# Kernel tuning notes

Measured on AMD Instinct MI355X. Metric: run time of the kernel, lower is better.

Reference implementation:

```python
import jax, jax.numpy as jnp
import numpy as np

E = 256  # embed_dim (hardcoded in source module)
H = 4    # n_head
D = E // H
SEQ = 32768


def setup_inputs() -> dict:
    key = jax.random.key(0)
    ks = jax.random.split(key, 5)
    x = jax.random.normal(ks[0], (SEQ, E), dtype=jnp.float32)
    in_proj_weight = jax.random.normal(ks[1], (3 * E, E), dtype=jnp.float32) * (1.0 / np.sqrt(E))
    in_proj_bias = jax.random.normal(ks[2], (3 * E,), dtype=jnp.float32) * 0.02
    out_proj_weight = jax.random.normal(ks[3], (E, E), dtype=jnp.float32) * (1.0 / np.sqrt(E))
    out_proj_bias = jax.random.normal(ks[4], (E,), dtype=jnp.float32) * 0.02
    return {
        "x": x,
        "in_proj_weight": in_proj_weight,
        "in_proj_bias": in_proj_bias,
        "out_proj_weight": out_proj_weight,
        "out_proj_bias": out_proj_bias,
    }


def reference(x, in_proj_weight, in_proj_bias, out_proj_weight, out_proj_bias):
    # QKV projections (q uses only the first token of x: single-query decode attention)
    Wq, Wk, Wv = in_proj_weight[:E], in_proj_weight[E:2 * E], in_proj_weight[2 * E:]
    bq, bk, bv = in_proj_bias[:E], in_proj_bias[E:2 * E], in_proj_bias[2 * E:]
    q = x[:1] @ Wq.T + bq            # [1, E]
    k = x @ Wk.T + bk                # [S, E]
    v = x @ Wv.T + bv                # [S, E]

    qh = q.reshape(H, D)             # [H, D] (single query)
    kh = k.reshape(-1, H, D)         # [S, H, D]
    vh = v.reshape(-1, H, D)         # [S, H, D]

    scale = 1.0 / np.sqrt(D).astype(np.float32)
    scores = jnp.einsum("hd,shd->hs", qh, kh) * scale   # [H, S]
    attn = jax.nn.softmax(scores, axis=-1)                # [H, S]
    ctx = jnp.einsum("hs,shd->hd", attn, vh)             # [H, D]

    out = ctx.reshape(1, E) @ out_proj_weight.T + out_proj_bias  # [1, E]
    return out
```

## Files before the change

### kernel.cpp

```cpp
#include <hip/hip_runtime.h>
#include <hip/hip_cooperative_groups.h>
namespace cg = cooperative_groups;

#define S 32768
#define NBLK 256


__device__ __forceinline__ float dot4(float4 a, float4 b) {
  return a.x * b.x + a.y * b.y + a.z * b.z + a.w * b.w;
}

__device__ __forceinline__ void phaseA(const float* __restrict__ x, const float* __restrict__ W,
                                       const float* __restrict__ inb, const float* __restrict__ Wout,
                                       float* __restrict__ kq, float* __restrict__ c4,
                                       float* __restrict__ M2, float* sh, int bid, int t) {
  const int lane = t & 63, w = t >> 6;
  if (bid < 16) {
    float* xs = sh;
    float* qls = sh + 256;
    float* red = sh + 320;
    const int h = bid >> 2, qt = bid & 3;
    if (t < 256) xs[t] = x[t];
    __syncthreads();
    const float4 xv = *(const float4*)&xs[lane * 4];
#pragma unroll
    for (int k = 0; k < 8; ++k) {
      const int eloc = w * 8 + k;
      const int row = h * 64 + eloc;
      float4 wv = *(const float4*)&W[(size_t)row * 256 + lane * 4];
      float p = dot4(wv, xv);
#pragma unroll
      for (int m = 1; m < 64; m <<= 1) p += __shfl_xor(p, m);
      if (lane == 0) qls[eloc] = p + inb[row];
    }
    __syncthreads();
    const int cl = t & 63, ds = t >> 6;
    float acc = 0.f;
#pragma unroll
    for (int d2 = 0; d2 < 8; ++d2) {
      const int d = ds * 8 + d2;
      acc += W[(size_t)(256 + h * 64 + d) * 256 + qt * 64 + cl] * qls[d];
    }
    red[ds * 64 + cl] = acc;
    __syncthreads();
    if (ds == 0) {
      float s = 0.f;
#pragma unroll
      for (int i = 0; i < 8; ++i) s += red[i * 64 + cl];
      kq[h * 256 + qt * 64 + cl] = s;
    }
    if (qt == 0 && t < 64) {
      float v = qls[t] * inb[256 + h * 64 + t];
#pragma unroll
      for (int m = 1; m < 64; m <<= 1) v += __shfl_xor(v, m);
      if (t == 0) c4[h] = v;
    }
  } else if (bid < 144) {
    float* wout_t = sh;
    const int b2 = bid - 16;
    const int tile = b2 >> 1, sub = b2 & 1;
    const int h = tile >> 4, e0 = (tile & 15) * 16 + sub * 8;
    {
      const int e = t >> 6, d = t & 63;
      wout_t[e * 64 + d] = Wout[(size_t)(e0 + e) * 256 + h * 64 + d];
    }
    __syncthreads();
    const int c = t & 255, eh = t >> 8;
    float acc[4] = {0.f, 0.f, 0.f, 0.f};
#pragma unroll 8
    for (int d = 0; d < 64; ++d) {
      const float wv = W[(size_t)(512 + h * 64 + d) * 256 + c];
#pragma unroll
      for (int e = 0; e < 4; ++e) acc[e] += wv * wout_t[(eh * 4 + e) * 64 + d];
    }
#pragma unroll
    for (int e = 0; e < 4; ++e)
      M2[(size_t)(e0 + eh * 4 + e) * 1024 + h * 256 + c] = acc[e];
  }
}

__device__ __forceinline__ float bscore(float4 xv, float4 kq0, float4 kq1, float4 kq2,
                                        float4 kq3, float c4v, int lane) {
  float p0 = dot4(xv, kq0), p1 = dot4(xv, kq1), p2 = dot4(xv, kq2), p3 = dot4(xv, kq3);
  const bool b1 = (lane & 2) != 0;
  float keep0 = b1 ? p2 : p0, send0 = b1 ? p0 : p2;
  keep0 += __shfl_xor(send0, 2);
  float keep1 = b1 ? p3 : p1, send1 = b1 ? p1 : p3;
  keep1 += __shfl_xor(send1, 2);
  const bool b0 = (lane & 1) != 0;
  float vv = b0 ? keep1 : keep0, sv = b0 ? keep0 : keep1;
  vv += __shfl_xor(sv, 1);
  vv += __shfl_xor(vv, 4);
  vv += __shfl_xor(vv, 8);
  vv += __shfl_xor(vv, 16);
  vv += __shfl_xor(vv, 32);
  return (vv + c4v) * 0.125f;
}

__device__ __forceinline__ void phaseB(const float* __restrict__ x, const float* __restrict__ kq,
                                       const float* __restrict__ c4, float* __restrict__ ypart,
                                       float* __restrict__ mpart, float* __restrict__ lpart,
                                       float* sh, int bid, int t) {
  float* yls = sh;
  float* sml = sh + 8192;
  float* sll = sh + 8224;
  const int lane = t & 63, w = t >> 6;
  const int hme = lane & 3;
  const float4 kq0 = *(const float4*)&kq[0 * 256 + lane * 4];
  const float4 kq1 = *(const float4*)&kq[1 * 256 + lane * 4];
  const float4 kq2 = *(const float4*)&kq[2 * 256 + lane * 4];
  const float4 kq3 = *(const float4*)&kq[3 * 256 + lane * 4];
  const float c4v = c4[hme];

  const int r0 = bid * 128 + w * 16;
  float4 xvA[8], xvB[8];
#pragma unroll
  for (int r = 0; r < 8; ++r)
    xvA[r] = *(const float4*)&x[(size_t)(r0 + r) * 256 + lane * 4];
#pragma unroll
  for (int r = 0; r < 8; ++r)
    xvB[r] = *(const float4*)&x[(size_t)(r0 + 8 + r) * 256 + lane * 4];

  float vA[8];
#pragma unroll
  for (int r = 0; r < 8; ++r) vA[r] = bscore(xvA[r], kq0, kq1, kq2, kq3, c4v, lane);
  float m = vA[0];
#pragma unroll
  for (int r = 1; r < 8; ++r) m = fmaxf(m, vA[r]);

  float l = 0.f;
  float4 a[4];
#pragma unroll
  for (int k = 0; k < 4; ++k) a[k] = (float4){0.f, 0.f, 0.f, 0.f};
#pragma unroll
  for (int r = 0; r < 8; ++r) {
    const float e0 = __expf(vA[r] - m);
    l += e0;
    const float e1 = __shfl_xor(e0, 1);
    const float e2 = __shfl_xor(e0, 2);
    const float e3 = __shfl_xor(e0, 3);
    a[0].x += e0 * xvA[r].x; a[0].y += e0 * xvA[r].y; a[0].z += e0 * xvA[r].z; a[0].w += e0 * xvA[r].w;
    a[1].x += e1 * xvA[r].x; a[1].y += e1 * xvA[r].y; a[1].z += e1 * xvA[r].z; a[1].w += e1 * xvA[r].w;
    a[2].x += e2 * xvA[r].x; a[2].y += e2 * xvA[r].y; a[2].z += e2 * xvA[r].z; a[2].w += e2 * xvA[r].w;
    a[3].x += e3 * xvA[r].x; a[3].y += e3 * xvA[r].y; a[3].z += e3 * xvA[r].z; a[3].w += e3 * xvA[r].w;
  }

  float vB[8];
#pragma unroll
  for (int r = 0; r < 8; ++r) vB[r] = bscore(xvB[r], kq0, kq1, kq2, kq3, c4v, lane);
  float mB = vB[0];
#pragma unroll
  for (int r = 1; r < 8; ++r) mB = fmaxf(mB, vB[r]);

  {
    const float mN = fmaxf(m, mB);
    const float fown = __expf(m - mN);
    l *= fown;
    const float f1 = __shfl_xor(fown, 1);
    const float f2 = __shfl_xor(fown, 2);
    const float f3 = __shfl_xor(fown, 3);
    a[0].x *= fown; a[0].y *= fown; a[0].z *= fown; a[0].w *= fown;
    a[1].x *= f1;   a[1].y *= f1;   a[1].z *= f1;   a[1].w *= f1;
    a[2].x *= f2;   a[2].y *= f2;   a[2].z *= f2;   a[2].w *= f2;
    a[3].x *= f3;   a[3].y *= f3;   a[3].z *= f3;   a[3].w *= f3;
    m = mN;
  }
#pragma unroll
  for (int r = 0; r < 8; ++r) {
    const float e0 = __expf(vB[r] - m);
    l += e0;
    const float e1 = __shfl_xor(e0, 1);
    const float e2 = __shfl_xor(e0, 2);
    const float e3 = __shfl_xor(e0, 3);
    a[0].x += e0 * xvB[r].x; a[0].y += e0 * xvB[r].y; a[0].z += e0 * xvB[r].z; a[0].w += e0 * xvB[r].w;
    a[1].x += e1 * xvB[r].x; a[1].y += e1 * xvB[r].y; a[1].z += e1 * xvB[r].z; a[1].w += e1 * xvB[r].w;
    a[2].x += e2 * xvB[r].x; a[2].y += e2 * xvB[r].y; a[2].z += e2 * xvB[r].z; a[2].w += e2 * xvB[r].w;
    a[3].x += e3 * xvB[r].x; a[3].y += e3 * xvB[r].y; a[3].z += e3 * xvB[r].z; a[3].w += e3 * xvB[r].w;
  }

  __syncthreads();
  if (lane < 4) { sml[w * 4 + lane] = m; sll[w * 4 + lane] = l; }
  __syncthreads();

#pragma unroll
  for (int k = 0; k < 4; ++k) {
    const int h = hme ^ k;
    float mb = sml[h];
#pragma unroll
    for (int i = 1; i < 8; ++i) mb = fmaxf(mb, sml[i * 4 + h]);
    const float f = __expf(sml[w * 4 + h] - mb);
    float4 av;
    av.x = a[k].x * f; av.y = a[k].y * f; av.z = a[k].z * f; av.w = a[k].w * f;
    *(float4*)&yls[w * 1024 + h * 256 + lane * 4] = av;
  }
  __syncthreads();

  if (t < 4) {
    float mb = sml[t];
#pragma unroll
    for (int i = 1; i < 8; ++i) mb = fmaxf(mb, sml[i * 4 + t]);
    float lb = 0.f;
#pragma unroll
    for (int i = 0; i < 8; ++i) lb += sll[i * 4 + t] * __expf(sml[i * 4 + t] - mb);
    mpart[t * NBLK + bid] = mb;
    lpart[t * NBLK + bid] = lb;
  }
  float* yp = &ypart[(size_t)bid * 1024];
#pragma unroll
  for (int o = t; o < 1024; o += 512) {
    float s = 0.f;
#pragma unroll
    for (int i = 0; i < 8; ++i) s += yls[i * 1024 + o];
    yp[o] = s;
  }
}

__device__ __forceinline__ void phaseC(const float* __restrict__ ypart, const float* __restrict__ mpart,
                                       const float* __restrict__ lpart, float* __restrict__ yv,
                                       float* sh, int bid, int t) {
  float* mred = sh;
  float* scales = sh + 256;
  float* lred = sh + 512;
  float* sred = sh + 768;
  const int h = bid >> 4;
  const int o0 = bid * 16;
  if (t < 256) mred[t] = mpart[h * 256 + t];
  __syncthreads();
  for (int s = 128; s > 0; s >>= 1) {
    if (t < s) mred[t] = fmaxf(mred[t], mred[t + s]);
    __syncthreads();
  }
  const float mg = mred[0];
  if (t < 256) {
    const float sc = __expf(mpart[h * 256 + t] - mg);
    scales[t] = sc;
    lred[t] = lpart[h * 256 + t] * sc;
  }
  __syncthreads();
  for (int s = 128; s > 0; s >>= 1) {
    if (t < s) lred[t] += lred[t + s];
    __syncthreads();
  }
  const float inv = 1.0f / lred[0];
  const int ol = t & 15, bg = t >> 4;
  float s = 0.f;
#pragma unroll
  for (int j = 0; j < 8; ++j) {
    const int b = bg * 8 + j;
    s += ypart[(size_t)b * 1024 + o0 + ol] * scales[b];
  }
  sred[bg * 16 + ol] = s;
  __syncthreads();
  if (t < 16) {
    float tot = 0.f;
#pragma unroll
    for (int g = 0; g < 32; ++g) tot += sred[g * 16 + t];
    yv[o0 + t] = tot * inv;
  }
}

__device__ __forceinline__ void phaseD(const float* __restrict__ M2, const float* __restrict__ yv,
                                       const float* __restrict__ Wout, const float* __restrict__ inb,
                                       const float* __restrict__ bout, float* __restrict__ out,
                                       float* sh, int bid, int t) {
  float* yls = sh;
  float* bvls = sh + 1024;
  float* smo = sh + 1280;
  for (int i = t; i < 1024; i += 512) yls[i] = yv[i];
  if (t < 256) bvls[t] = inb[512 + t];
  __syncthreads();
  const int og = t >> 5, seg = t & 31;
  const int e = bid * 16 + og;
  float acc = 0.f;
  const float4* m4 = (const float4*)&M2[(size_t)e * 1024 + seg * 32];
  const float4* y4 = (const float4*)&yls[seg * 32];
#pragma unroll
  for (int j = 0; j < 8; ++j) acc += dot4(m4[j], y4[j]);
  if (seg < 8) {
    const float4* w4 = (const float4*)&Wout[(size_t)e * 256 + seg * 32];
    const float4* b4 = (const float4*)&bvls[seg * 32];
#pragma unroll
    for (int j = 0; j < 8; ++j) acc += dot4(w4[j], b4[j]);
  }
  smo[og * 32 + seg] = acc;
  __syncthreads();
  if (t < 16) {
    float s = bout[bid * 16 + t];
#pragma unroll
    for (int i = 0; i < 32; ++i) s += smo[t * 32 + i];
    out[bid * 16 + t] = s;
  }
}

__global__ void __launch_bounds__(512, 2) mha_coop(const float* __restrict__ x,
                                                   const float* __restrict__ W,
                                                   const float* __restrict__ inb,
                                                   const float* __restrict__ Wout,
                                                   const float* __restrict__ bout,
                                                   float* __restrict__ out,
                                                   float* __restrict__ ws) {
  __shared__ __align__(16) float sh[8448];
  float* c4 = ws;
  float* kq = ws + 64;
  float* mpart = ws + 1088;
  float* lpart = ws + 2112;
  float* yv = ws + 3136;
  float* M2 = ws + 4160;
  float* ypart = ws + 266304;
  const int t = threadIdx.x, bid = blockIdx.x;
  cg::grid_group grid = cg::this_grid();
  phaseA(x, W, inb, Wout, kq, c4, M2, sh, bid, t);
  grid.sync();
  phaseB(x, kq, c4, ypart, mpart, lpart, sh, bid, t);
  grid.sync();
  if (bid < 64) phaseC(ypart, mpart, lpart, yv, sh, bid, t);
  grid.sync();
  if (bid < 16) phaseD(M2, yv, Wout, inb, bout, out, sh, bid, t);
}

__global__ void __launch_bounds__(512) fb_A(const float* __restrict__ x, const float* __restrict__ W,
                                            const float* __restrict__ inb, const float* __restrict__ Wout,
                                            float* __restrict__ ws) {
  __shared__ __align__(16) float sh[832];
  phaseA(x, W, inb, Wout, ws + 64, ws, ws + 4160, sh, blockIdx.x, threadIdx.x);
}
__global__ void __launch_bounds__(512) fb_B(const float* __restrict__ x, float* __restrict__ ws) {
  __shared__ __align__(16) float sh[8256];
  phaseB(x, ws + 64, ws, ws + 266304, ws + 1088, ws + 2112, sh, blockIdx.x, threadIdx.x);
}
__global__ void __launch_bounds__(512) fb_C(float* __restrict__ ws) {
  __shared__ __align__(16) float sh[1280];
  phaseC(ws + 266304, ws + 1088, ws + 2112, ws + 3136, sh, blockIdx.x, threadIdx.x);
}
__global__ void __launch_bounds__(512) fb_D(const float* __restrict__ Wout, const float* __restrict__ inb,
                                            const float* __restrict__ bout, float* __restrict__ out,
                                            float* __restrict__ ws) {
  __shared__ __align__(16) float sh[1792];
  phaseD(ws + 4160, ws + 3136, Wout, inb, bout, out, sh, blockIdx.x, threadIdx.x);
}

extern "C" void kernel_launch(void* const* d_in, const int* in_sizes, int n_in,
                              void* d_out, int out_size, void* d_ws, size_t ws_size,
                              hipStream_t stream) {
  const float* x = (const float*)d_in[0];
  const float* W = (const float*)d_in[1];
  const float* inb = (const float*)d_in[2];
  const float* Wout = (const float*)d_in[3];
  const float* bout = (const float*)d_in[4];
  float* out = (float*)d_out;
  float* ws = (float*)d_ws;

  int dev = 0;
  (void)hipGetDevice(&dev);
  int coopAttr = 0, ncu = 0, occ = 0;
  bool coop = (hipDeviceGetAttribute(&coopAttr, hipDeviceAttributeCooperativeLaunch, dev) == hipSuccess) &&
              coopAttr != 0;
  coop = coop &&
         (hipDeviceGetAttribute(&ncu, hipDeviceAttributeMultiprocessorCount, dev) == hipSuccess);
  coop = coop &&
         (hipOccupancyMaxActiveBlocksPerMultiprocessor(&occ, mha_coop, 512, 0) == hipSuccess);
  coop = coop && (occ * ncu >= NBLK);

  if (coop) {
    void* args[] = {(void*)&x, (void*)&W, (void*)&inb, (void*)&Wout,
                    (void*)&bout, (void*)&out, (void*)&ws};
    if (hipLaunchCooperativeKernel((const void*)mha_coop, dim3(NBLK), dim3(512),
                                   args, 0, stream) == hipSuccess)
      return;
  }
  fb_A<<<144, 512, 0, stream>>>(x, W, inb, Wout, ws);
  fb_B<<<NBLK, 512, 0, stream>>>(x, ws);
  fb_C<<<64, 512, 0, stream>>>(ws);
  fb_D<<<16, 512, 0, stream>>>(Wout, inb, bout, out, ws);
}
```

Measured before the change: 32.08 us.

## Replace grid-wide syncs with counter-based dataflow signaling and last-arrival tickets

Drops the three cooperative grid.sync barriers and replaces them with atomic counters: blocks spin only on the kq counter before phase B, and later phases are run by whichever blocks arrive last (ticket scheme), so early finishers exit. Blocks not needed for kq/c4 issue their x loads before waiting, overlapping the load with phase A. The bias term Wout·bv+bout is precomputed in phase A by extra blocks, which shortens phase D. A memset of the counters is added per launch, and correctness now depends on every block being co-resident and on the spin loops.

New measurement: 36.03 us. 1.12x slower.

```diff
diff --git a/kernel.cpp b/kernel.cpp
--- a/kernel.cpp
+++ b/kernel.cpp
@@ -1,81 +1,126 @@
 #include <hip/hip_runtime.h>
-#include <hip/hip_cooperative_groups.h>
-namespace cg = cooperative_groups;
 
 #define S 32768
 #define NBLK 256
-
+#define WS_C4   0
+#define WS_KQ   64
+#define WS_MP   1088
+#define WS_LP   2112
+#define WS_YV   3136
+#define WS_B2   4160
+#define WS_M2   4416
+#define WS_YP   266560
+#define WS_CNT  528704
 
 __device__ __forceinline__ float dot4(float4 a, float4 b) {
   return a.x * b.x + a.y * b.y + a.z * b.z + a.w * b.w;
 }
 
-__device__ __forceinline__ void phaseA(const float* __restrict__ x, const float* __restrict__ W,
-                                       const float* __restrict__ inb, const float* __restrict__ Wout,
-                                       float* __restrict__ kq, float* __restrict__ c4,
-                                       float* __restrict__ M2, float* sh, int bid, int t) {
+__device__ __forceinline__ void signal_done(int* p) {
+  __threadfence();
+  __syncthreads();
+  if (threadIdx.x == 0) atomicAdd(p, 1);
+}
+__device__ __forceinline__ void spin_until(int* p, int target) {
+  if (threadIdx.x == 0) {
+    while (atomicAdd(p, 0) < target) __builtin_amdgcn_s_sleep(2);
+  }
+  __syncthreads();
+  __threadfence();
+}
+__device__ __forceinline__ int take_ticket(int* p, int* shi) {
+  __threadfence();
+  __syncthreads();
+  if (threadIdx.x == 0) *shi = atomicAdd(p, 1);
+  __syncthreads();
+  return *shi;
+}
+
+__device__ __forceinline__ void phaseA_kq(const float* __restrict__ x, const float* __restrict__ W,
+                                          const float* __restrict__ inb, float* __restrict__ kq,
+                                          float* __restrict__ c4, float* sh, int bid, int t) {
+  float* xs = sh;
+  float* qls = sh + 256;
+  float* red = sh + 320;
   const int lane = t & 63, w = t >> 6;
-  if (bid < 16) {
-    float* xs = sh;
-    float* qls = sh + 256;
-    float* red = sh + 320;
-    const int h = bid >> 2, qt = bid & 3;
-    if (t < 256) xs[t] = x[t];
-    __syncthreads();
-    const float4 xv = *(const float4*)&xs[lane * 4];
-#pragma unroll
-    for (int k = 0; k < 8; ++k) {
-      const int eloc = w * 8 + k;
-      const int row = h * 64 + eloc;
-      float4 wv = *(const float4*)&W[(size_t)row * 256 + lane * 4];
-      float p = dot4(wv, xv);
-#pragma unroll
-      for (int m = 1; m < 64; m <<= 1) p += __shfl_xor(p, m);
-      if (lane == 0) qls[eloc] = p + inb[row];
-    }
-    __syncthreads();
-    const int cl = t & 63, ds = t >> 6;
-    float acc = 0.f;
-#pragma unroll
-    for (int d2 = 0; d2 < 8; ++d2) {
-      const int d = ds * 8 + d2;
-      acc += W[(size_t)(256 + h * 64 + d) * 256 + qt * 64 + cl] * qls[d];
-    }
-    red[ds * 64 + cl] = acc;
-    __syncthreads();
-    if (ds == 0) {
-      float s = 0.f;
-#pragma unroll
-      for (int i = 0; i < 8; ++i) s += red[i * 64 + cl];
-      kq[h * 256 + qt * 64 + cl] = s;
-    }
-    if (qt == 0 && t < 64) {
-      float v = qls[t] * inb[256 + h * 64 + t];
-#pragma unroll
-      for (int m = 1; m < 64; m <<= 1) v += __shfl_xor(v, m);
-      if (t == 0) c4[h] = v;
-    }
-  } else if (bid < 144) {
-    float* wout_t = sh;
-    const int b2 = bid - 16;
-    const int tile = b2 >> 1, sub = b2 & 1;
-    const int h = tile >> 4, e0 = (tile & 15) * 16 + sub * 8;
-    {
-      const int e = t >> 6, d = t & 63;
-      wout_t[e * 64 + d] = Wout[(size_t)(e0 + e) * 256 + h * 64 + d];
-    }
-    __syncthreads();
-    const int c = t & 255, eh = t >> 8;
-    float acc[4] = {0.f, 0.f, 0.f, 0.f};
+  const int h = bid >> 2, qt = bid & 3;
+  if (t < 256) xs[t] = x[t];
+  __syncthreads();
+  const float4 xv = *(const float4*)&xs[lane * 4];
+#pragma unroll
+  for (int k = 0; k < 8; ++k) {
+    const int eloc = w * 8 + k;
+    const int row = h * 64 + eloc;
+    float4 wv = *(const float4*)&W[(size_t)row * 256 + lane * 4];
+    float p = dot4(wv, xv);
+#pragma unroll
+    for (int m = 1; m < 64; m <<= 1) p += __shfl_xor(p, m);
+    if (lane == 0) qls[eloc] = p + inb[row];
+  }
+  __syncthreads();
+  const int cl = t & 63, ds = t >> 6;
+  float acc = 0.f;
+#pragma unroll
+  for (int d2 = 0; d2 < 8; ++d2) {
+    const int d = ds * 8 + d2;
+    acc += W[(size_t)(256 + h * 64 + d) * 256 + qt * 64 + cl] * qls[d];
+  }
+  red[ds * 64 + cl] = acc;
+  __syncthreads();
+  if (ds == 0) {
+    float s = 0.f;
+#pragma unroll
+    for (int i = 0; i < 8; ++i) s += red[i * 64 + cl];
+    kq[h * 256 + qt * 64 + cl] = s;
+  }
+  if (qt == 0 && t < 64) {
+    float v = qls[t] * inb[256 + h * 64 + t];
+#pragma unroll
+    for (int m = 1; m < 64; m <<= 1) v += __shfl_xor(v, m);
+    if (t == 0) c4[h] = v;
+  }
+}
+
+__device__ __forceinline__ void phaseA_m2(const float* __restrict__ W, const float* __restrict__ Wout,
+                                          float* __restrict__ M2, float* sh, int b2, int t) {
+  float* wout_t = sh;
+  const int tile = b2 >> 1, sub = b2 & 1;
+  const int h = tile >> 4, e0 = (tile & 15) * 16 + sub * 8;
+  {
+    const int e = t >> 6, d = t & 63;
+    wout_t[e * 64 + d] = Wout[(size_t)(e0 + e) * 256 + h * 64 + d];
+  }
+  __syncthreads();
+  const int c = t & 255, eh = t >> 8;
+  float acc[4] = {0.f, 0.f, 0.f, 0.f};
 #pragma unroll 8
-    for (int d = 0; d < 64; ++d) {
-      const float wv = W[(size_t)(512 + h * 64 + d) * 256 + c];
-#pragma unroll
-      for (int e = 0; e < 4; ++e) acc[e] += wv * wout_t[(eh * 4 + e) * 64 + d];
-    }
-#pragma unroll
-    for (int e = 0; e < 4; ++e)
-      M2[(size_t)(e0 + eh * 4 + e) * 1024 + h * 256 + c] = acc[e];
+  for (int d = 0; d < 64; ++d) {
+    const float wv = W[(size_t)(512 + h * 64 + d) * 256 + c];
+#pragma unroll
+    for (int e = 0; e < 4; ++e) acc[e] += wv * wout_t[(eh * 4 + e) * 64 + d];
+  }
+#pragma unroll
+  for (int e = 0; e < 4; ++e)
+    M2[(size_t)(e0 + eh * 4 + e) * 1024 + h * 256 + c] = acc[e];
+}
+
+__device__ __forceinline__ void phaseA_b2(const float* __restrict__ Wout, const float* __restrict__ inb,
+                                          const float* __restrict__ bout, float* __restrict__ bias2,
+                                          float* sh, int b, int t) {
+  float* red = sh;
+  const int og = t >> 5, seg = t & 31;
+  const int e = b * 16 + og;
+  float acc = 0.f;
+#pragma unroll
+  for (int j = 0; j < 8; ++j)
+    acc += Wout[(size_t)e * 256 + seg * 8 + j] * inb[512 + seg * 8 + j];
+  red[og * 32 + seg] = acc;
+  __syncthreads();
+  if (t < 16) {
+    float s = bout[b * 16 + t];
+#pragma unroll
+    for (int i = 0; i < 32; ++i) s += red[t * 32 + i];
+    bias2[b * 16 + t] = s;
   }
 }
 
@@ -97,10 +142,10 @@
   return (vv + c4v) * 0.125f;
 }
 
-__device__ __forceinline__ void phaseB(const float* __restrict__ x, const float* __restrict__ kq,
-                                       const float* __restrict__ c4, float* __restrict__ ypart,
-                                       float* __restrict__ mpart, float* __restrict__ lpart,
-                                       float* sh, int bid, int t) {
+__device__ __forceinline__ void phaseB_core(const float4* xvA, const float4* xvB,
+                                            const float* __restrict__ kq, const float* __restrict__ c4,
+                                            float* __restrict__ ypart, float* __restrict__ mpart,
+                                            float* __restrict__ lpart, float* sh, int bid, int t) {
   float* yls = sh;
   float* sml = sh + 8192;
   float* sll = sh + 8224;
@@ -111,15 +156,6 @@
   const float4 kq2 = *(const float4*)&kq[2 * 256 + lane * 4];
   const float4 kq3 = *(const float4*)&kq[3 * 256 + lane * 4];
   const float c4v = c4[hme];
-
-  const int r0 = bid * 128 + w * 16;
-  float4 xvA[8], xvB[8];
-#pragma unroll
-  for (int r = 0; r < 8; ++r)
-    xvA[r] = *(const float4*)&x[(size_t)(r0 + r) * 256 + lane * 4];
-#pragma unroll
-  for (int r = 0; r < 8; ++r)
-    xvB[r] = *(const float4*)&x[(size_t)(r0 + 8 + r) * 256 + lane * 4];
 
   float vA[8];
 #pragma unroll
@@ -260,14 +296,11 @@
 }
 
 __device__ __forceinline__ void phaseD(const float* __restrict__ M2, const float* __restrict__ yv,
-                                       const float* __restrict__ Wout, const float* __restrict__ inb,
-                                       const float* __restrict__ bout, float* __restrict__ out,
+                                       const float* __restrict__ bias2, float* __restrict__ out,
                                        float* sh, int bid, int t) {
   float* yls = sh;
-  float* bvls = sh + 1024;
-  float* smo = sh + 1280;
+  float* smo = sh + 1024;
   for (int i = t; i < 1024; i += 512) yls[i] = yv[i];
-  if (t < 256) bvls[t] = inb[512 + t];
   __syncthreads();
   const int og = t >> 5, seg = t & 31;
   const int e = bid * 16 + og;
@@ -276,23 +309,17 @@
   const float4* y4 = (const float4*)&yls[seg * 32];
 #pragma unroll
   for (int j = 0; j < 8; ++j) acc += dot4(m4[j], y4[j]);
-  if (seg < 8) {
-    const float4* w4 = (const float4*)&Wout[(size_t)e * 256 + seg * 32];
-    const float4* b4 = (const float4*)&bvls[seg * 32];
-#pragma unroll
-    for (int j = 0; j < 8; ++j) acc += dot4(w4[j], b4[j]);
-  }
   smo[og * 32 + seg] = acc;
   __syncthreads();
   if (t < 16) {
-    float s = bout[bid * 16 + t];
+    float s = bias2[bid * 16 + t];
 #pragma unroll
     for (int i = 0; i < 32; ++i) s += smo[t * 32 + i];
     out[bid * 16 + t] = s;
   }
 }
 
-__global__ void __launch_bounds__(512, 2) mha_coop(const float* __restrict__ x,
+__global__ void __launch_bounds__(512, 1) mha_coop(const float* __restrict__ x,
                                                    const float* __restrict__ W,
                                                    const float* __restrict__ inb,
                                                    const float* __restrict__ Wout,
@@ -300,43 +327,93 @@
                                                    float* __restrict__ out,
                                                    float* __restrict__ ws) {
   __shared__ __align__(16) float sh[8448];
-  float* c4 = ws;
-  float* kq = ws + 64;
-  float* mpart = ws + 1088;
-  float* lpart = ws + 2112;
-  float* yv = ws + 3136;
-  float* M2 = ws + 4160;
-  float* ypart = ws + 266304;
+  __shared__ int shi;
   const int t = threadIdx.x, bid = blockIdx.x;
-  cg::grid_group grid = cg::this_grid();
-  phaseA(x, W, inb, Wout, kq, c4, M2, sh, bid, t);
-  grid.sync();
-  phaseB(x, kq, c4, ypart, mpart, lpart, sh, bid, t);
-  grid.sync();
-  if (bid < 64) phaseC(ypart, mpart, lpart, yv, sh, bid, t);
-  grid.sync();
-  if (bid < 16) phaseD(M2, yv, Wout, inb, bout, out, sh, bid, t);
+  const int lane = t & 63, w = t >> 6;
+  int* cnt = (int*)(ws + WS_CNT);
+  float* c4 = ws + WS_C4;
+  float* kq = ws + WS_KQ;
+  float* mpart = ws + WS_MP;
+  float* lpart = ws + WS_LP;
+  float* yv = ws + WS_YV;
+  float* bias2 = ws + WS_B2;
+  float* M2 = ws + WS_M2;
+  float* ypart = ws + WS_YP;
+
+  const int r0 = bid * 128 + w * 16;
+  float4 xvA[8], xvB[8];
+
+  if (bid >= 16) {
+#pragma unroll
+    for (int r = 0; r < 8; ++r)
+      xvA[r] = *(const float4*)&x[(size_t)(r0 + r) * 256 + lane * 4];
+#pragma unroll
+    for (int r = 0; r < 8; ++r)
+      xvB[r] = *(const float4*)&x[(size_t)(r0 + 8 + r) * 256 + lane * 4];
+  }
+
+  if (bid < 16) {
+    phaseA_kq(x, W, inb, kq, c4, sh, bid, t);
+    signal_done(&cnt[0]);
+#pragma unroll
+    for (int r = 0; r < 8; ++r)
+      xvA[r] = *(const float4*)&x[(size_t)(r0 + r) * 256 + lane * 4];
+#pragma unroll
+    for (int r = 0; r < 8; ++r)
+      xvB[r] = *(const float4*)&x[(size_t)(r0 + 8 + r) * 256 + lane * 4];
+  } else if (bid < 144) {
+    phaseA_m2(W, Wout, M2, sh, bid - 16, t);
+    signal_done(&cnt[1]);
+  } else if (bid < 160) {
+    phaseA_b2(Wout, inb, bout, bias2, sh, bid - 144, t);
+    signal_done(&cnt[1]);
+  }
+
+  spin_until(&cnt[0], 16);
+  phaseB_core(xvA, xvB, kq, c4, ypart, mpart, lpart, sh, bid, t);
+
+  const int tk = take_ticket(&cnt[2], &shi);
+  if (tk < NBLK - 64) return;
+  spin_until(&cnt[2], NBLK);
+  phaseC(ypart, mpart, lpart, yv, sh, tk - (NBLK - 64), t);
+
+  const int t2 = take_ticket(&cnt[3], &shi);
+  if (t2 < 48) return;
+  spin_until(&cnt[3], 64);
+  spin_until(&cnt[1], 144);
+  phaseD(M2, yv, bias2, out, sh, t2 - 48, t);
 }
 
 __global__ void __launch_bounds__(512) fb_A(const float* __restrict__ x, const float* __restrict__ W,
                                             const float* __restrict__ inb, const float* __restrict__ Wout,
-                                            float* __restrict__ ws) {
+                                            const float* __restrict__ bout, float* __restrict__ ws) {
   __shared__ __align__(16) float sh[832];
-  phaseA(x, W, inb, Wout, ws + 64, ws, ws + 4160, sh, blockIdx.x, threadIdx.x);
+  const int bid = blockIdx.x, t = threadIdx.x;
+  if (bid < 16) phaseA_kq(x, W, inb, ws + WS_KQ, ws + WS_C4, sh, bid, t);
+  else if (bid < 144) phaseA_m2(W, Wout, ws + WS_M2, sh, bid - 16, t);
+  else if (bid < 160) phaseA_b2(Wout, inb, bout, ws + WS_B2, sh, bid - 144, t);
 }
 __global__ void __launch_bounds__(512) fb_B(const float* __restrict__ x, float* __restrict__ ws) {
   __shared__ __align__(16) float sh[8256];
-  phaseB(x, ws + 64, ws, ws + 266304, ws + 1088, ws + 2112, sh, blockIdx.x, threadIdx.x);
+  const int bid = blockIdx.x, t = threadIdx.x;
+  const int lane = t & 63, w = t >> 6;
+  const int r0 = bid * 128 + w * 16;
+  float4 xvA[8], xvB[8];
+#pragma unroll
+  for (int r = 0; r < 8; ++r)
+    xvA[r] = *(const float4*)&x[(size_t)(r0 + r) * 256 + lane * 4];
+#pragma unroll
+  for (int r = 0; r < 8; ++r)
+    xvB[r] = *(const float4*)&x[(size_t)(r0 + 8 + r) * 256 + lane * 4];
+  phaseB_core(xvA, xvB, ws + WS_KQ, ws + WS_C4, ws + WS_YP, ws + WS_MP, ws + WS_LP, sh, bid, t);
 }
 __global__ void __launch_bounds__(512) fb_C(float* __restrict__ ws) {
   __shared__ __align__(16) float sh[1280];
-  phaseC(ws + 266304, ws + 1088, ws + 2112, ws + 3136, sh, blockIdx.x, threadIdx.x);
-}
-__global__ void __launch_bounds__(512) fb_D(const float* __restrict__ Wout, const float* __restrict__ inb,
-                                            const float* __restrict__ bout, float* __restrict__ out,
-                                            float* __restrict__ ws) {
-  __shared__ __align__(16) float sh[1792];
-  phaseD(ws + 4160, ws + 3136, Wout, inb, bout, out, sh, blockIdx.x, threadIdx.x);
+  phaseC(ws + WS_YP, ws + WS_MP, ws + WS_LP, ws + WS_YV, sh, blockIdx.x, threadIdx.x);
+}
+__global__ void __launch_bounds__(512) fb_D(float* __restrict__ out, float* __restrict__ ws) {
+  __shared__ __align__(16) float sh[1536];
+  phaseD(ws + WS_M2, ws + WS_YV, ws + WS_B2, out, sh, blockIdx.x, threadIdx.x);
 }
 
 extern "C" void kernel_launch(void* const* d_in, const int* in_sizes, int n_in,
@@ -350,6 +427,8 @@
   float* out = (float*)d_out;
   float* ws = (float*)d_ws;
 
+  hipMemsetAsync((void*)(ws + WS_CNT), 0, 16, stream);
+
   int dev = 0;
   (void)hipGetDevice(&dev);
   int coopAttr = 0, ncu = 0, occ = 0;
@@ -368,8 +447,8 @@
                                    args, 0, stream) == hipSuccess)
       return;
   }
-  fb_A<<<144, 512, 0, stream>>>(x, W, inb, Wout, ws);
+  fb_A<<<160, 512, 0, stream>>>(x, W, inb, Wout, bout, ws);
   fb_B<<<NBLK, 512, 0, stream>>>(x, ws);
   fb_C<<<64, 512, 0, stream>>>(ws);
-  fb_D<<<16, 512, 0, stream>>>(Wout, inb, bout, out, ws);
-}
+  fb_D<<<16, 512, 0, stream>>>(out, ws);
+}
```
